# Performance work log

Measured on AMD Instinct MI355X. Metric: run time of the kernel, lower is better.

Reference implementation:

```python
import jax, jax.numpy as jnp
import numpy as np

EMBED = 1024
HEADS = 16
HEAD_DIM = EMBED // HEADS


def setup_inputs() -> dict:
    key = jax.random.key(0)
    ks = jax.random.split(key, 10)
    s = 1.0 / np.sqrt(EMBED)
    inp = {
        "x": jax.random.normal(ks[0], (4, 2048, EMBED), dtype=jnp.float32),
        "mask": jax.random.randint(ks[1], (4, 2048), 0, 2, dtype=jnp.int32),
        "Wq": jax.random.uniform(ks[2], (EMBED, EMBED), jnp.float32, -s, s),
        "bq": jax.random.uniform(ks[3], (EMBED,), jnp.float32, -s, s),
        "Wk": jax.random.uniform(ks[4], (EMBED, EMBED), jnp.float32, -s, s),
        "bk": jax.random.uniform(ks[5], (EMBED,), jnp.float32, -s, s),
        "Wv": jax.random.uniform(ks[6], (EMBED, EMBED), jnp.float32, -s, s),
        "bv": jax.random.uniform(ks[7], (EMBED,), jnp.float32, -s, s),
        "Wo": jax.random.uniform(ks[8], (EMBED, EMBED), jnp.float32, -s, s),
        "bo": jax.random.uniform(ks[9], (EMBED,), jnp.float32, -s, s),
    }
    return inp


def reference(x, mask, Wq, bq, Wk, bk, Wv, bv, Wo, bo):
    B, S, E = x.shape
    scale = np.sqrt(HEAD_DIM).astype(np.float32)

    def split_heads(t):  # [B,S,E] -> [B,H,S,D]
        return t.reshape(B, S, HEADS, HEAD_DIM).transpose(0, 2, 1, 3)

    Q = split_heads(x @ Wq.T + bq)
    K = split_heads(x @ Wk.T + bk)
    V = split_heads(x @ Wv.T + bv)

    scores = jnp.einsum("bhqd,bhkd->bhqk", Q, K) / scale  # [B,H,S,S]
    # mask [B,S] broadcast over heads and query dim (key-padding mask)
    scores = jnp.where(mask[:, None, None, :] == 0, -jnp.inf, scores)
    weights = jax.nn.softmax(scores, axis=-1)
    out = jnp.einsum("bhqk,bhkd->bhqd", weights, V)  # [B,H,S,D]
    out = out.transpose(0, 2, 1, 3).reshape(B, S, E)
    return out @ Wo.T + bo
```

## Files before the change

kernel.cpp:

```cpp
#include <hip/hip_runtime.h>

#define BATCH 4
#define SEQ   2048
#define EMBED 1024
#define HEADS 16
#define HDIM  64
#define NTOK  (BATCH*SEQ)

typedef __attribute__((ext_vector_type(8)))  short short8;
typedef __attribute__((ext_vector_type(4)))  float f32x4;
typedef __attribute__((ext_vector_type(16))) float f32x16;

static __device__ __forceinline__ unsigned short f2bf(float f) {
    union { float f; unsigned u; } v; v.f = f;
    return (unsigned short)((v.u + 0x7FFFu + ((v.u >> 16) & 1u)) >> 16);
}
static __device__ __forceinline__ unsigned cvtpk(float lo, float hi) {
    unsigned r;
    asm("v_cvt_pk_bf16_f32 %0, %1, %2" : "=v"(r) : "v"(lo), "v"(hi));
    return r;
}
static __device__ __forceinline__ void gload_lds16(const unsigned short* g, unsigned short* l) {
    __builtin_amdgcn_global_load_lds(
        (__attribute__((address_space(1))) void*)g,
        (__attribute__((address_space(3))) void*)l, 16, 0, 0);
}

#define SCQ 0.180336880f

__global__ void cast_all(const float* __restrict__ x,
                         const float* __restrict__ w0, const float* __restrict__ w1,
                         const float* __restrict__ w2, const float* __restrict__ w3,
                         unsigned short* __restrict__ xb,
                         unsigned short* __restrict__ wb)
{
    const int bid = blockIdx.x;
    const float* src;
    unsigned short* dst;
    int i;
    if (bid < 4096) {
        src = x; dst = xb; i = (bid * 256 + threadIdx.x) * 8;
    } else {
        const int wz = (bid - 4096) >> 9;
        const float* ws[4] = {w0, w1, w2, w3};
        src = ws[wz];
        dst = wb + (size_t)wz * (EMBED * EMBED);
        i = (((bid - 4096) & 511) * 256 + threadIdx.x) * 8;
    }
    float4 a = *(const float4*)(src + i);
    float4 b = *(const float4*)(src + i + 4);
    union { int4 v; unsigned short u[8]; } pk;
    pk.u[0] = f2bf(a.x); pk.u[1] = f2bf(a.y); pk.u[2] = f2bf(a.z); pk.u[3] = f2bf(a.w);
    pk.u[4] = f2bf(b.x); pk.u[5] = f2bf(b.y); pk.u[6] = f2bf(b.z); pk.u[7] = f2bf(b.w);
    *(int4*)(dst + i) = pk.v;
}

__global__ __launch_bounds__(256, 2)
void gemm_qkv(const unsigned short* __restrict__ Xb,
              const unsigned short* __restrict__ Wall,
              const float* __restrict__ bq, const float* __restrict__ bk,
              const float* __restrict__ bv,
              unsigned short* __restrict__ Qw, unsigned short* __restrict__ Kw,
              unsigned short* __restrict__ VtG)
{
    __shared__ unsigned short Ws[3][128][32];
    __shared__ unsigned short Xs[128][32];

    const int tid  = threadIdx.x;
    const int bx   = blockIdx.x, by = blockIdx.y;
    const int f0   = (by >> 3) * 128;
    const int t0   = ((bx << 3) | (by & 7)) * 128;
    const int lane = tid & 63, m = lane & 15, quad = lane >> 4;
    const int wid  = tid >> 6;
    const int wf   = (wid & 1) * 64;
    const int wt   = (wid >> 1) * 64;

    const int r    = tid >> 2, cc = tid & 3, sw = (tid >> 4) & 3;
    const int gcol = (cc ^ sw) << 3;
    const unsigned short* Xp = Xb + (size_t)(t0 + r) * EMBED + gcol;
    const unsigned short* Wp = Wall + (size_t)(f0 + r) * EMBED + gcol;
    unsigned short* XsL = &Xs[0][0] + tid * 8;
    unsigned short* WsL = &Ws[0][0][0] + tid * 8;

    const int qs = (quad ^ ((m >> 2) & 3)) << 3;

    f32x4 aq[4][4] = {}, ak[4][4] = {}, av[4][4] = {};

    for (int k0 = 0; k0 < EMBED; k0 += 32) {
        __syncthreads();
        gload_lds16(Xp + k0,              XsL);
        gload_lds16(Xp + k0 + 64 * EMBED, XsL + 2048);
#pragma unroll
        for (int z = 0; z < 3; ++z) {
            const unsigned short* wz = Wp + (size_t)z * EMBED * EMBED + k0;
            gload_lds16(wz,              WsL + z * 4096);
            gload_lds16(wz + 64 * EMBED, WsL + z * 4096 + 2048);
        }
        __syncthreads();

        short8 bf4[4];
#pragma unroll
        for (int nb = 0; nb < 4; ++nb)
            bf4[nb] = *(const short8*)&Xs[wt + nb * 16 + m][qs];

#pragma unroll
        for (int z = 0; z < 3; ++z) {
            short8 af[4];
#pragma unroll
            for (int mb = 0; mb < 4; ++mb)
                af[mb] = *(const short8*)&Ws[z][wf + mb * 16 + m][qs];
            f32x4 (&acc)[4][4] = (z == 0) ? aq : (z == 1) ? ak : av;
#pragma unroll
            for (int mb = 0; mb < 4; ++mb)
#pragma unroll
                for (int nb = 0; nb < 4; ++nb)
                    acc[mb][nb] = __builtin_amdgcn_mfma_f32_16x16x32_bf16(
                        af[mb], bf4[nb], acc[mb][nb], 0, 0, 0);
        }
    }

#pragma unroll
    for (int mb = 0; mb < 4; ++mb) {
        const int feat = f0 + wf + mb * 16 + quad * 4;
        float4 bv4 = *(const float4*)&bq[feat];
#pragma unroll
        for (int nb = 0; nb < 4; ++nb) {
            const int tok = t0 + wt + nb * 16 + m;
            ushort4 pk;
            pk.x = f2bf((aq[mb][nb][0] + bv4.x) * SCQ);
            pk.y = f2bf((aq[mb][nb][1] + bv4.y) * SCQ);
            pk.z = f2bf((aq[mb][nb][2] + bv4.z) * SCQ);
            pk.w = f2bf((aq[mb][nb][3] + bv4.w) * SCQ);
            *(ushort4*)(Qw + (size_t)tok * EMBED + feat) = pk;
        }
    }
#pragma unroll
    for (int mb = 0; mb < 4; ++mb) {
        const int feat = f0 + wf + mb * 16 + quad * 4;
        float4 bv4 = *(const float4*)&bk[feat];
#pragma unroll
        for (int nb = 0; nb < 4; ++nb) {
            const int tok = t0 + wt + nb * 16 + m;
            ushort4 pk;
            pk.x = f2bf(ak[mb][nb][0] + bv4.x);
            pk.y = f2bf(ak[mb][nb][1] + bv4.y);
            pk.z = f2bf(ak[mb][nb][2] + bv4.z);
            pk.w = f2bf(ak[mb][nb][3] + bv4.w);
            *(ushort4*)(Kw + (size_t)tok * EMBED + feat) = pk;
        }
    }
    {
        const int h = (f0 + wf) >> 6;
#pragma unroll
        for (int nb = 0; nb < 4; ++nb) {
            const int tok = t0 + wt + nb * 16 + m;
            const int b   = tok >> 11;
            const int s   = tok & (SEQ - 1);
            const size_t base = ((size_t)(b * HEADS + h) * HDIM) * SEQ + s;
#pragma unroll
            for (int mb = 0; mb < 4; ++mb) {
                const int feat  = f0 + wf + mb * 16 + quad * 4;
                const int dbase = mb * 16 + quad * 4;
                float4 bv4 = *(const float4*)&bv[feat];
                VtG[base + (size_t)(dbase + 0) * SEQ] = f2bf(av[mb][nb][0] + bv4.x);
                VtG[base + (size_t)(dbase + 1) * SEQ] = f2bf(av[mb][nb][1] + bv4.y);
                VtG[base + (size_t)(dbase + 2) * SEQ] = f2bf(av[mb][nb][2] + bv4.z);
                VtG[base + (size_t)(dbase + 3) * SEQ] = f2bf(av[mb][nb][3] + bv4.w);
            }
        }
    }
}

__global__ __launch_bounds__(256, 4)
void attn_mfma(const unsigned short* __restrict__ Qb,
               const unsigned short* __restrict__ Kb,
               const unsigned short* __restrict__ VtG,
               const int* __restrict__ mask,
               unsigned short* __restrict__ Ob)
{
    __shared__ unsigned short Ks[2][64][72];
    __shared__ unsigned short Vs[2][64][72];

    const int tid  = threadIdx.x;
    const int lin  = (blockIdx.x & 7) * 128 + (blockIdx.x >> 3);
    const int qb   = lin & 15;
    const int h    = (lin >> 4) & 15;
    const int b    = lin >> 8;
    const int wid  = tid >> 6, lane = tid & 63;
    const int q32  = lane & 31, hi = lane >> 5;
    const int tb   = b * SEQ;
    const int q    = qb * 128 + wid * 32 + q32;

    const unsigned short* qrow = Qb + (size_t)(tb + q) * EMBED + h * HDIM;
    short8 qf[4];
#pragma unroll
    for (int st = 0; st < 4; ++st)
        qf[st] = *(const short8*)(qrow + st * 16 + hi * 8);

    short8 mqf = {0, 0, 0, 0, 0, 0, 0, 0};
    mqf[0] = hi ? (short)0 : (short)0xC480;

    f32x16 o0, o1, z16;
#pragma unroll
    for (int i = 0; i < 16; ++i) { z16[i] = 0.f; }
    o0 = z16; o1 = z16;
    float lr = 0.f;

    const int sr = tid >> 2, sc = (tid & 3) * 16;
    const unsigned short* kSrc = Kb + (size_t)(tb + sr) * EMBED + h * HDIM + sc;
    const unsigned short* vSrc = VtG + ((size_t)(b * HEADS + h) * HDIM + sr) * SEQ + sc;
    const int* mrow = mask + b * SEQ;

    auto compute = [&](const unsigned short (*Kc)[72],
                       const unsigned short (*Vc)[72], int mva, int mvb) {
        __builtin_amdgcn_s_setprio(1);
        short8 mkfa = {0, 0, 0, 0, 0, 0, 0, 0};
        short8 mkfb = {0, 0, 0, 0, 0, 0, 0, 0};
        mkfa[0] = (hi == 0 && mva == 0) ? (short)0x3F80 : (short)0;
        mkfb[0] = (hi == 0 && mvb == 0) ? (short)0x3F80 : (short)0;
#pragma unroll
        for (int kb = 0; kb < 2; ++kb) {
            f32x16 s = __builtin_amdgcn_mfma_f32_32x32x16_bf16(
                kb ? mkfb : mkfa, mqf, z16, 0, 0, 0);
#pragma unroll
            for (int st = 0; st < 4; ++st) {
                short8 kf = *(const short8*)&Kc[kb * 32 + q32][st * 16 + hi * 8];
                s = __builtin_amdgcn_mfma_f32_32x32x16_bf16(kf, qf[st], s, 0, 0, 0);
            }

            float p[16];
#pragma unroll
            for (int i = 0; i < 16; ++i) p[i] = __builtin_amdgcn_exp2f(s[i]);

            lr += (((p[0] + p[1]) + (p[2] + p[3])) + ((p[4] + p[5]) + (p[6] + p[7])))
                + (((p[8] + p[9]) + (p[10] + p[11])) + ((p[12] + p[13]) + (p[14] + p[15])));

            unsigned D[8];
#pragma unroll
            for (int j = 0; j < 8; ++j) D[j] = cvtpk(p[2 * j], p[2 * j + 1]);

#pragma unroll
            for (int cl = 0; cl < 2; ++cl) {
                unsigned x0 = D[4 * cl + 0], x1 = D[4 * cl + 1];
                unsigned x2 = D[4 * cl + 2], x3 = D[4 * cl + 3];
                asm("v_permlane32_swap_b32 %0, %1" : "+v"(x0), "+v"(x2));
                asm("v_permlane32_swap_b32 %0, %1" : "+v"(x1), "+v"(x3));
                union { uint4 u; short8 s8; } fr;
                fr.u.x = x0; fr.u.y = x1; fr.u.z = x2; fr.u.w = x3;

                const int kcol = kb * 32 + cl * 16 + hi * 8;
                short8 vf0 = *(const short8*)&Vc[q32][kcol];
                short8 vf1 = *(const short8*)&Vc[32 + q32][kcol];
                o0 = __builtin_amdgcn_mfma_f32_32x32x16_bf16(vf0, fr.s8, o0, 0, 0, 0);
                o1 = __builtin_amdgcn_mfma_f32_32x32x16_bf16(vf1, fr.s8, o1, 0, 0, 0);
            }
        }
        __builtin_amdgcn_s_setprio(0);
    };

    int mva_c, mvb_c;
    {
        int4 kv0 = *(const int4*)(kSrc);
        int4 kv1 = *(const int4*)(kSrc + 8);
        int4 vv0 = *(const int4*)(vSrc);
        int4 vv1 = *(const int4*)(vSrc + 8);
        mva_c = mrow[q32];
        mvb_c = mrow[32 + q32];
        *(int4*)&Ks[0][sr][sc]     = kv0;
        *(int4*)&Ks[0][sr][sc + 8] = kv1;
        *(int4*)&Vs[0][sr][sc]     = vv0;
        *(int4*)&Vs[0][sr][sc + 8] = vv1;
        __syncthreads();
    }

    int cur = 0;
    for (int kt = 0; kt + 64 < SEQ; kt += 64) {
        const unsigned short* kp = kSrc + (size_t)(kt + 64) * EMBED;
        int4 kv0 = *(const int4*)(kp);
        int4 kv1 = *(const int4*)(kp + 8);
        int4 vv0 = *(const int4*)(vSrc + kt + 64);
        int4 vv1 = *(const int4*)(vSrc + kt + 64 + 8);
        const int mva_n = mrow[kt + 64 + q32];
        const int mvb_n = mrow[kt + 96 + q32];

        compute(Ks[cur], Vs[cur], mva_c, mvb_c);

        __syncthreads();
        const int nxt = cur ^ 1;
        *(int4*)&Ks[nxt][sr][sc]     = kv0;
        *(int4*)&Ks[nxt][sr][sc + 8] = kv1;
        *(int4*)&Vs[nxt][sr][sc]     = vv0;
        *(int4*)&Vs[nxt][sr][sc + 8] = vv1;
        __syncthreads();
        mva_c = mva_n; mvb_c = mvb_n; cur = nxt;
    }
    compute(Ks[cur], Vs[cur], mva_c, mvb_c);

    const float lrt = lr + __shfl_xor(lr, 32);
    const float inv = 1.0f / lrt;
    unsigned short* orow = Ob + (size_t)(tb + q) * EMBED + h * HDIM;
#pragma unroll
    for (int db = 0; db < 2; ++db) {
        const f32x16& oo = db ? o1 : o0;
#pragma unroll
        for (int qg = 0; qg < 4; ++qg) {
            ushort4 pk;
            pk.x = f2bf(oo[qg * 4 + 0] * inv);
            pk.y = f2bf(oo[qg * 4 + 1] * inv);
            pk.z = f2bf(oo[qg * 4 + 2] * inv);
            pk.w = f2bf(oo[qg * 4 + 3] * inv);
            *(ushort4*)(orow + db * 32 + qg * 8 + hi * 4) = pk;
        }
    }
}

__global__ __launch_bounds__(256, 2)
void gemm_o(const unsigned short* __restrict__ W, const unsigned short* __restrict__ X,
            const float* __restrict__ bias, float* __restrict__ Cout)
{
    __shared__ unsigned short Ws[128][32];
    __shared__ unsigned short Xs[128][32];

    const int tid  = threadIdx.x;
    const int bx   = blockIdx.x, by = blockIdx.y;
    const int f0   = (by >> 3) * 128;
    const int t0   = ((bx << 3) | (by & 7)) * 128;
    const int lane = tid & 63, m = lane & 15, quad = lane >> 4;
    const int wid  = tid >> 6;
    const int wf   = (wid & 1) * 64;
    const int wt   = (wid >> 1) * 64;

    const int r    = tid >> 2, cc = tid & 3, sw = (tid >> 4) & 3;
    const int gcol = (cc ^ sw) << 3;
    const unsigned short* Wp = W + (size_t)(f0 + r) * EMBED + gcol;
    const unsigned short* Xp = X + (size_t)(t0 + r) * EMBED + gcol;
    unsigned short* WsL = &Ws[0][0] + tid * 8;
    unsigned short* XsL = &Xs[0][0] + tid * 8;

    const int qs = (quad ^ ((m >> 2) & 3)) << 3;

    f32x4 acc[4][4] = {};

    for (int k0 = 0; k0 < EMBED; k0 += 32) {
        __syncthreads();
        gload_lds16(Wp + k0,              WsL);
        gload_lds16(Wp + k0 + 64 * EMBED, WsL + 2048);
        gload_lds16(Xp + k0,              XsL);
        gload_lds16(Xp + k0 + 64 * EMBED, XsL + 2048);
        __syncthreads();

        short8 af[4], bf4[4];
#pragma unroll
        for (int mb = 0; mb < 4; ++mb)
            af[mb] = *(const short8*)&Ws[wf + mb * 16 + m][qs];
#pragma unroll
        for (int nb = 0; nb < 4; ++nb)
            bf4[nb] = *(const short8*)&Xs[wt + nb * 16 + m][qs];
#pragma unroll
        for (int mb = 0; mb < 4; ++mb)
#pragma unroll
            for (int nb = 0; nb < 4; ++nb)
                acc[mb][nb] = __builtin_amdgcn_mfma_f32_16x16x32_bf16(
                    af[mb], bf4[nb], acc[mb][nb], 0, 0, 0);
    }

#pragma unroll
    for (int mb = 0; mb < 4; ++mb) {
        const int feat = f0 + wf + mb * 16 + quad * 4;
        float4 bv4 = *(const float4*)&bias[feat];
#pragma unroll
        for (int nb = 0; nb < 4; ++nb) {
            const int tok = t0 + wt + nb * 16 + m;
            float4 st;
            st.x = acc[mb][nb][0] + bv4.x;
            st.y = acc[mb][nb][1] + bv4.y;
            st.z = acc[mb][nb][2] + bv4.z;
            st.w = acc[mb][nb][3] + bv4.w;
            *(float4*)(Cout + (size_t)tok * EMBED + feat) = st;
        }
    }
}

extern "C" void kernel_launch(void* const* d_in, const int* in_sizes, int n_in,
                              void* d_out, int out_size, void* d_ws, size_t ws_size,
                              hipStream_t stream)
{
    const float* x    = (const float*)d_in[0];
    const int*   mask = (const int*)  d_in[1];
    const float* Wq   = (const float*)d_in[2];
    const float* bq   = (const float*)d_in[3];
    const float* Wk   = (const float*)d_in[4];
    const float* bk   = (const float*)d_in[5];
    const float* Wv   = (const float*)d_in[6];
    const float* bv   = (const float*)d_in[7];
    const float* Wo   = (const float*)d_in[8];
    const float* bo   = (const float*)d_in[9];
    float* out = (float*)d_out;

    const size_t NE = (size_t)NTOK * EMBED;
    const size_t WE = (size_t)EMBED * EMBED;
    unsigned short* Xb  = (unsigned short*)d_ws;
    unsigned short* Wqb = Xb + NE;
    unsigned short* Wob = Wqb + 3 * WE;
    unsigned short* Qw  = Wob + WE;
    unsigned short* Kw  = Qw + NE;
    unsigned short* VtG = Kw + NE;
    unsigned short* Ow  = Xb;

    cast_all<<<4096 + 2048, 256, 0, stream>>>(x, Wq, Wk, Wv, Wo, Xb, Wqb);

    gemm_qkv<<<dim3(8, 64), 256, 0, stream>>>(Xb, Wqb, bq, bk, bv, Qw, Kw, VtG);

    attn_mfma<<<BATCH * HEADS * (SEQ / 128), 256, 0, stream>>>(Qw, Kw, VtG, mask, Ow);

    gemm_o<<<dim3(8, 64), 256, 0, stream>>>(Wob, Ow, bo, out);
}
```

Before: 276.2 us.

## Permute V transpose layout to drop permlane swaps and precompute mask bits

The QKV projection now writes V^T with sequence indices bit-permuted (bits 2 and 3 swapped), so the P fragments from the score MFMA can feed the PV MFMA directly without v_permlane32_swap. The key-padding mask is loaded once per thread into a 64-bit bitmask before the loop instead of two global loads per tile. The two score MFMA chains are issued back to back so both can be in flight together. This spreads the layout change across two kernels and adds a 64-iteration mask load prologue.

```diff
diff --git a/kernel.cpp b/kernel.cpp
--- a/kernel.cpp
+++ b/kernel.cpp
@@ -156,7 +156,8 @@
             const int tok = t0 + wt + nb * 16 + m;
             const int b   = tok >> 11;
             const int s   = tok & (SEQ - 1);
-            const size_t base = ((size_t)(b * HEADS + h) * HDIM) * SEQ + s;
+            const int sp  = (s & ~12) | ((s & 4) << 1) | ((s & 8) >> 1);
+            const size_t base = ((size_t)(b * HEADS + h) * HDIM) * SEQ + sp;
 #pragma unroll
             for (int mb = 0; mb < 4; ++mb) {
                 const int feat  = f0 + wf + mb * 16 + quad * 4;
@@ -197,6 +198,12 @@
     for (int st = 0; st < 4; ++st)
         qf[st] = *(const short8*)(qrow + st * 16 + hi * 8);
 
+    const int* mrow = mask + b * SEQ;
+    unsigned long long mbits = 0;
+#pragma unroll 8
+    for (int j = 0; j < 64; ++j)
+        mbits |= (unsigned long long)(mrow[j * 32 + q32] != 0 ? 1 : 0) << j;
+
     short8 mqf = {0, 0, 0, 0, 0, 0, 0, 0};
     mqf[0] = hi ? (short)0 : (short)0xC480;
 
@@ -209,28 +216,31 @@
     const int sr = tid >> 2, sc = (tid & 3) * 16;
     const unsigned short* kSrc = Kb + (size_t)(tb + sr) * EMBED + h * HDIM + sc;
     const unsigned short* vSrc = VtG + ((size_t)(b * HEADS + h) * HDIM + sr) * SEQ + sc;
-    const int* mrow = mask + b * SEQ;
 
     auto compute = [&](const unsigned short (*Kc)[72],
-                       const unsigned short (*Vc)[72], int mva, int mvb) {
+                       const unsigned short (*Vc)[72], int jb) {
         __builtin_amdgcn_s_setprio(1);
         short8 mkfa = {0, 0, 0, 0, 0, 0, 0, 0};
         short8 mkfb = {0, 0, 0, 0, 0, 0, 0, 0};
-        mkfa[0] = (hi == 0 && mva == 0) ? (short)0x3F80 : (short)0;
-        mkfb[0] = (hi == 0 && mvb == 0) ? (short)0x3F80 : (short)0;
-#pragma unroll
-        for (int kb = 0; kb < 2; ++kb) {
-            f32x16 s = __builtin_amdgcn_mfma_f32_32x32x16_bf16(
-                kb ? mkfb : mkfa, mqf, z16, 0, 0, 0);
+        mkfa[0] = (hi == 0 && !((mbits >> jb) & 1))       ? (short)0x3F80 : (short)0;
+        mkfb[0] = (hi == 0 && !((mbits >> (jb + 1)) & 1)) ? (short)0x3F80 : (short)0;
+
+        f32x16 s[2];
+        s[0] = __builtin_amdgcn_mfma_f32_32x32x16_bf16(mkfa, mqf, z16, 0, 0, 0);
+        s[1] = __builtin_amdgcn_mfma_f32_32x32x16_bf16(mkfb, mqf, z16, 0, 0, 0);
+#pragma unroll
+        for (int kb = 0; kb < 2; ++kb)
 #pragma unroll
             for (int st = 0; st < 4; ++st) {
                 short8 kf = *(const short8*)&Kc[kb * 32 + q32][st * 16 + hi * 8];
-                s = __builtin_amdgcn_mfma_f32_32x32x16_bf16(kf, qf[st], s, 0, 0, 0);
+                s[kb] = __builtin_amdgcn_mfma_f32_32x32x16_bf16(kf, qf[st], s[kb], 0, 0, 0);
             }
 
+#pragma unroll
+        for (int kb = 0; kb < 2; ++kb) {
             float p[16];
 #pragma unroll
-            for (int i = 0; i < 16; ++i) p[i] = __builtin_amdgcn_exp2f(s[i]);
+            for (int i = 0; i < 16; ++i) p[i] = __builtin_amdgcn_exp2f(s[kb][i]);
 
             lr += (((p[0] + p[1]) + (p[2] + p[3])) + ((p[4] + p[5]) + (p[6] + p[7])))
                 + (((p[8] + p[9]) + (p[10] + p[11])) + ((p[12] + p[13]) + (p[14] + p[15])));
@@ -241,12 +251,9 @@
 
 #pragma unroll
             for (int cl = 0; cl < 2; ++cl) {
-                unsigned x0 = D[4 * cl + 0], x1 = D[4 * cl + 1];
-                unsigned x2 = D[4 * cl + 2], x3 = D[4 * cl + 3];
-                asm("v_permlane32_swap_b32 %0, %1" : "+v"(x0), "+v"(x2));
-                asm("v_permlane32_swap_b32 %0, %1" : "+v"(x1), "+v"(x3));
                 union { uint4 u; short8 s8; } fr;
-                fr.u.x = x0; fr.u.y = x1; fr.u.z = x2; fr.u.w = x3;
+                fr.u.x = D[4 * cl + 0]; fr.u.y = D[4 * cl + 1];
+                fr.u.z = D[4 * cl + 2]; fr.u.w = D[4 * cl + 3];
 
                 const int kcol = kb * 32 + cl * 16 + hi * 8;
                 short8 vf0 = *(const short8*)&Vc[q32][kcol];
@@ -258,14 +265,11 @@
         __builtin_amdgcn_s_setprio(0);
     };
 
-    int mva_c, mvb_c;
     {
         int4 kv0 = *(const int4*)(kSrc);
         int4 kv1 = *(const int4*)(kSrc + 8);
         int4 vv0 = *(const int4*)(vSrc);
         int4 vv1 = *(const int4*)(vSrc + 8);
-        mva_c = mrow[q32];
-        mvb_c = mrow[32 + q32];
         *(int4*)&Ks[0][sr][sc]     = kv0;
         *(int4*)&Ks[0][sr][sc + 8] = kv1;
         *(int4*)&Vs[0][sr][sc]     = vv0;
@@ -280,10 +284,8 @@
         int4 kv1 = *(const int4*)(kp + 8);
         int4 vv0 = *(const int4*)(vSrc + kt + 64);
         int4 vv1 = *(const int4*)(vSrc + kt + 64 + 8);
-        const int mva_n = mrow[kt + 64 + q32];
-        const int mvb_n = mrow[kt + 96 + q32];
-
-        compute(Ks[cur], Vs[cur], mva_c, mvb_c);
+
+        compute(Ks[cur], Vs[cur], kt >> 5);
 
         __syncthreads();
         const int nxt = cur ^ 1;
@@ -292,9 +294,9 @@
         *(int4*)&Vs[nxt][sr][sc]     = vv0;
         *(int4*)&Vs[nxt][sr][sc + 8] = vv1;
         __syncthreads();
-        mva_c = mva_n; mvb_c = mvb_n; cur = nxt;
-    }
-    compute(Ks[cur], Vs[cur], mva_c, mvb_c);
+        cur = nxt;
+    }
+    compute(Ks[cur], Vs[cur], (SEQ - 64) >> 5);
 
     const float lrt = lr + __shfl_xor(lr, 32);
     const float inv = 1.0f / lrt;
```

Result: faster. 267.8 us (-3.0%).
